# Kernel tuning notes

Hardware: AMD Instinct MI355X
Metric: run time of the kernel (lower is better)

Reference implementation:

```python
import jax, jax.numpy as jnp
import numpy as np

N, IN, HID, OUT, HEADS = 50000, 128, 128, 16, 4
EL, EG = 800000, 200000
NEG_SLOPE = 0.2


def setup_inputs() -> dict:
    key = jax.random.key(0)
    ks = jax.random.split(key, 24)
    def gn(k, shape, fan_in):
        return (jax.random.normal(k, shape, jnp.float32) / np.sqrt(fan_in)).astype(jnp.float32)
    inp = {}
    inp['x'] = jax.random.normal(ks[0], (N, IN), jnp.float32)
    inp['local_edge_index'] = jax.random.randint(ks[1], (2, EL), 0, N, jnp.int64 if jax.config.jax_enable_x64 else jnp.int32)
    inp['global_edge_index'] = jax.random.randint(ks[2], (2, EG), 0, N, jnp.int64 if jax.config.jax_enable_x64 else jnp.int32)
    # local_processor: Linear(IN, HID)
    inp['W1'] = gn(ks[3], (IN, HID), IN); inp['b1'] = jnp.zeros((HID,), jnp.float32)
    # GCNConv(HID, HID): weight + bias
    inp['Wg'] = gn(ks[4], (HID, HID), HID); inp['bg'] = jnp.zeros((HID,), jnp.float32)
    # GATConv(HID, HID, heads=4, concat=False): lin to HEADS*HID, att vectors, bias of size HID
    inp['Wa'] = gn(ks[5], (HID, HEADS * HID), HID)
    inp['att_src'] = gn(ks[6], (HEADS, HID), HID)
    inp['att_dst'] = gn(ks[7], (HEADS, HID), HID)
    inp['ba'] = jnp.zeros((HID,), jnp.float32)
    # hierarchical_pool: Linear(2*HID, HID)
    inp['Wp'] = gn(ks[8], (2 * HID, HID), 2 * HID); inp['bp'] = jnp.zeros((HID,), jnp.float32)
    # classifier: Linear(HID, HID//2) -> ReLU -> Linear(HID//2, OUT)
    inp['Wc1'] = gn(ks[9], (HID, HID // 2), HID); inp['bc1'] = jnp.zeros((HID // 2,), jnp.float32)
    inp['Wc2'] = gn(ks[10], (HID // 2, OUT), HID // 2); inp['bc2'] = jnp.zeros((OUT,), jnp.float32)
    # uncertainty_head: Linear(HID, OUT)
    inp['Wu'] = gn(ks[11], (HID, OUT), HID); inp['bu'] = jnp.zeros((OUT,), jnp.float32)
    return inp


def _add_self_loops(ei, n):
    loop = jnp.arange(n, dtype=ei.dtype)
    return jnp.concatenate([ei[0], loop]), jnp.concatenate([ei[1], loop])


def gcn_conv(x, ei, W, b):
    n = x.shape[0]
    xw = x @ W                                        # [N, HID]
    src, dst = _add_self_loops(ei, n)
    deg = jax.ops.segment_sum(jnp.ones_like(dst, dtype=xw.dtype), dst, num_segments=n)
    dinv = jax.lax.rsqrt(jnp.maximum(deg, 1e-12))     # deg >= 1 thanks to self-loops
    norm = dinv[src] * dinv[dst]                      # [E+N]
    msg = xw[src] * norm[:, None]                     # gather + scale
    return jax.ops.segment_sum(msg, dst, num_segments=n) + b


def gat_conv(x, ei, W, att_src, att_dst, b):
    n = x.shape[0]
    h, c = att_src.shape
    xw = (x @ W).reshape(n, h, c)                     # [N, H, C]
    a_s = jnp.einsum('nhc,hc->nh', xw, att_src)       # [N, H]
    a_d = jnp.einsum('nhc,hc->nh', xw, att_dst)
    src, dst = _add_self_loops(ei, n)
    e = jax.nn.leaky_relu(a_s[src] + a_d[dst], NEG_SLOPE)   # [E+N, H]
    emax = jax.ops.segment_max(e, dst, num_segments=n)      # stable edge-softmax per dst
    ee = jnp.exp(e - emax[dst])
    denom = jax.ops.segment_sum(ee, dst, num_segments=n)
    alpha = ee / (denom[dst] + 1e-16)                        # [E+N, H]
    out = jax.ops.segment_sum(xw[src] * alpha[:, :, None], dst, num_segments=n)  # [N,H,C]
    return out.mean(axis=1) + b                              # concat=False -> head mean


def reference(x, local_edge_index, global_edge_index, W1, b1, Wg, bg, Wa, att_src, att_dst, ba, Wp, bp, Wc1, bc1, Wc2, bc2, Wu, bu):
    x_local = jax.nn.relu(x @ W1 + b1)                       # dropout is identity in eval
    x_lg = jax.nn.relu(gcn_conv(x_local, local_edge_index, Wg, bg))
    x_gg = jax.nn.relu(gat_conv(x_local, global_edge_index, Wa, att_src, att_dst, ba))
    x_comb = jnp.concatenate([x_lg, x_gg], axis=1)           # [N, 2*HID]
    x_pooled = jax.nn.relu(x_comb @ Wp + bp)
    x_final = x_pooled.mean(axis=0, keepdims=True)           # batch=None path
    prediction = jax.nn.relu(x_final @ Wc1 + bc1) @ Wc2 + bc2
    uncertainty = jax.nn.sigmoid(x_final @ Wu + bu)
    return prediction, uncertainty
```

## Files before the change

kernel.cpp:

```cpp
#include <hip/hip_runtime.h>
#include <hip/hip_bf16.h>

#define N_NODES 50000
#define F_IN 128
#define HID 128
#define N_OUT 16
#define HEADS 4
#define EL 800000
#define EG 200000
#define NEG_SLOPE 0.2f
#define NB 196
#define GB 391

typedef short bf16x8 __attribute__((ext_vector_type(8)));
typedef float f32x4 __attribute__((ext_vector_type(4)));
typedef float f32x2 __attribute__((ext_vector_type(2)));

static __device__ __forceinline__ float lrelu(float x) {
    return x > 0.f ? x : NEG_SLOPE * x;
}
static __device__ __forceinline__ unsigned short f2b(float f) {
    __hip_bfloat16 h = __float2bfloat16(f);
    return *reinterpret_cast<unsigned short*>(&h);
}
static __device__ __forceinline__ unsigned char f2fp8(float f) {
    unsigned pk = __builtin_amdgcn_cvt_pk_fp8_f32(f, f, 0, false);
    return (unsigned char)(pk & 0xFF);
}
static __device__ __forceinline__ f32x2 fp8x2_to_f32(unsigned u) {
    return __builtin_amdgcn_cvt_pk_f32_fp8((int)u, false);
}
static __device__ __forceinline__ float rdlane_f(float v, int l) {
    return __int_as_float(__builtin_amdgcn_readlane(__float_as_int(v), l));
}

__global__ __launch_bounds__(256) void conv_hist(
    const float* __restrict__ W1, unsigned short* __restrict__ W1t,
    const float* __restrict__ Wg, unsigned short* __restrict__ Wgt,
    const float* __restrict__ Wa, unsigned short* __restrict__ Wat,
    const float* __restrict__ Wp, unsigned short* __restrict__ Wpt,
    const int* __restrict__ ldst, const int* __restrict__ gdst, int* __restrict__ ghist)
{
    int b = blockIdx.x, t = threadIdx.x;
    if (b < 64) {
        int idx = b * 256 + t;
        int k = idx >> 7, n = idx & 127;
        W1t[n * 128 + k] = f2b(W1[idx]);
    } else if (b < 128) {
        int idx = (b - 64) * 256 + t;
        int k = idx >> 7, n = idx & 127;
        Wgt[n * 128 + k] = f2b(Wg[idx]);
    } else if (b < 384) {
        int idx = (b - 128) * 256 + t;
        int k = idx >> 9, n = idx & 511;
        Wat[(size_t)n * 128 + k] = f2b(Wa[idx]);
    } else if (b < 512) {
        int idx = (b - 384) * 256 + t;
        int k = idx >> 7, n = idx & 127;
        Wpt[(size_t)n * 256 + k] = f2b(Wp[idx]);
    } else {
        __shared__ int lh[NB];
        int blk = b - 512;
        bool loc = blk < 196;
        const int* dstp = loc ? ldst : gdst;
        int nE = loc ? EL : EG;
        int* gh = ghist + (loc ? 0 : NB);
        int start = (loc ? blk : blk - 196) * 4096;
        if (t < NB) lh[t] = 0;
        __syncthreads();
        #pragma unroll
        for (int i = 0; i < 16; i++) {
            int e = start + i * 256 + t;
            if (e < nE) atomicAdd(&lh[dstp[e] >> 8], 1);
        }
        __syncthreads();
        if (t < NB && lh[t]) atomicAdd(&gh[t], lh[t]);
    }
}

__global__ __launch_bounds__(256) void scan_gemmx(
    const int* __restrict__ ghist, int* __restrict__ bbase, int* __restrict__ gcur,
    const float* __restrict__ A, const unsigned short* __restrict__ Bt,
    const float* __restrict__ bias, unsigned short* __restrict__ out, int M)
{
    __shared__ unsigned short As[128 * 128];
    __shared__ unsigned short Bs[128 * 128];
    int tid = threadIdx.x;
    if (blockIdx.x < 2) {
        int* s = (int*)As;
        int g = blockIdx.x, t = tid;
        int v = (t < NB) ? ghist[g * NB + t] : 0;
        s[t] = v;
        __syncthreads();
        for (int off = 1; off < 256; off <<= 1) {
            int u = (t >= off) ? s[t - off] : 0;
            __syncthreads();
            s[t] += u;
            __syncthreads();
        }
        if (t < NB) {
            bbase[g * (NB + 1) + t] = s[t] - v;
            gcur[g * NB + t] = s[t] - v;
        }
        if (t == NB - 1) bbase[g * (NB + 1) + NB] = s[t];
        return;
    }
    int lane = tid & 63, w = tid >> 6;
    int wr = w >> 1, wc = w & 1;
    int l16 = lane & 15, lhi = lane >> 4;
    int m0 = (blockIdx.x - 2) * 128;
    f32x4 acc[4][4] = {};
    #pragma unroll
    for (int i = 0; i < 8; i++) {
        int u = tid + i * 256;
        int row = u >> 4, e0 = (u & 15) << 3;
        int sw = e0 ^ ((row & 7) << 3);
        int gr = m0 + row;
        unsigned short pb[8] = {};
        if (gr < M) {
            float4 a0 = *(const float4*)(A + (size_t)gr * 128 + e0);
            float4 a1 = *(const float4*)(A + (size_t)gr * 128 + e0 + 4);
            pb[0] = f2b(a0.x); pb[1] = f2b(a0.y); pb[2] = f2b(a0.z); pb[3] = f2b(a0.w);
            pb[4] = f2b(a1.x); pb[5] = f2b(a1.y); pb[6] = f2b(a1.z); pb[7] = f2b(a1.w);
        }
        *(bf16x8*)(As + row * 128 + sw) = *(bf16x8*)pb;
        bf16x8 vb = *(const bf16x8*)(Bt + (size_t)row * 128 + e0);
        *(bf16x8*)(Bs + row * 128 + sw) = vb;
    }
    __syncthreads();
    #pragma unroll
    for (int kk = 0; kk < 4; kk++) {
        int ke = kk * 32 + lhi * 8;
        bf16x8 af[4], bfr[4];
        #pragma unroll
        for (int m = 0; m < 4; m++) {
            int r = wr * 64 + m * 16 + l16;
            af[m] = *(const bf16x8*)(As + r * 128 + (ke ^ ((r & 7) << 3)));
        }
        #pragma unroll
        for (int n = 0; n < 4; n++) {
            int r = wc * 64 + n * 16 + l16;
            bfr[n] = *(const bf16x8*)(Bs + r * 128 + (ke ^ ((r & 7) << 3)));
        }
        #pragma unroll
        for (int m = 0; m < 4; m++)
            #pragma unroll
            for (int n = 0; n < 4; n++)
                acc[m][n] = __builtin_amdgcn_mfma_f32_16x16x32_bf16(af[m], bfr[n], acc[m][n], 0, 0, 0);
    }
    #pragma unroll
    for (int m = 0; m < 4; m++) {
        #pragma unroll
        for (int r = 0; r < 4; r++) {
            int row_g = m0 + wr * 64 + m * 16 + lhi * 4 + r;
            if (row_g >= M) continue;
            #pragma unroll
            for (int n = 0; n < 4; n++) {
                int col_g = wc * 64 + n * 16 + l16;
                float v = fmaxf(acc[m][n][r] + bias[col_g], 0.f);
                out[(size_t)row_g * 128 + col_g] = f2b(v);
            }
        }
    }
}

__global__ __launch_bounds__(256) void part_gw5(
    const unsigned short* __restrict__ A, const unsigned short* __restrict__ Wgt,
    const unsigned short* __restrict__ Wat,
    unsigned char* __restrict__ xw_g8, unsigned char* __restrict__ xw_a8, int M,
    const float* __restrict__ atts, const float* __restrict__ attd,
    float* __restrict__ a_s, float* __restrict__ a_d,
    const int* __restrict__ lsrc, const int* __restrict__ ldst,
    const int* __restrict__ gsrc, const int* __restrict__ gdst,
    int* __restrict__ gcur, unsigned* __restrict__ ebuf_l, unsigned* __restrict__ ebuf_g)
{
    __shared__ unsigned short As[128 * 128];
    __shared__ unsigned short Bs[128 * 128];
    __shared__ float sas[128], sad[128];
    int tid = threadIdx.x;
    if (blockIdx.x >= GB) {
        int* lhist = (int*)As;
        int* lbase = ((int*)As) + 256;
        int blk = blockIdx.x - GB, t = tid;
        bool loc = blk < 196;
        const int* srcp = loc ? lsrc : gsrc;
        const int* dstp = loc ? ldst : gdst;
        int nE = loc ? EL : EG;
        unsigned* ebuf = loc ? ebuf_l : ebuf_g;
        int* cur = gcur + (loc ? 0 : NB);
        int start = (loc ? blk : blk - 196) * 4096;
        if (t < NB) lhist[t] = 0;
        __syncthreads();
        unsigned pk[16];
        #pragma unroll
        for (int i = 0; i < 16; i++) {
            int e = start + i * 256 + t;
            if (e < nE) {
                unsigned d = (unsigned)dstp[e];
                pk[i] = (d << 16) | (unsigned)srcp[e];
                atomicAdd(&lhist[d >> 8], 1);
            } else pk[i] = 0xFFFFFFFFu;
        }
        __syncthreads();
        if (t < NB) lbase[t] = atomicAdd(&cur[t], lhist[t]);
        __syncthreads();
        if (t < NB) lhist[t] = 0;
        __syncthreads();
        #pragma unroll
        for (int i = 0; i < 16; i++) {
            unsigned b = pk[i] >> 24;
            if (b < NB) {
                int r = atomicAdd(&lhist[b], 1);
                ebuf[lbase[b] + r] = pk[i];
            }
        }
        return;
    }
    int lane = tid & 63, w = tid >> 6;
    int wr = w >> 1, wc = w & 1;
    int l16 = lane & 15, lhi = lane >> 4;
    int m0 = blockIdx.x * 128;
    #pragma unroll
    for (int i = 0; i < 8; i++) {
        int u = tid + i * 256;
        int row = u >> 4, e0 = (u & 15) << 3;
        int sw = e0 ^ ((row & 7) << 3);
        bf16x8 va = {};
        int gr = m0 + row;
        if (gr < M) va = *(const bf16x8*)(A + (size_t)gr * 128 + e0);
        *(bf16x8*)(As + row * 128 + sw) = va;
    }
    for (int p = 0; p < 5; p++) {
        const unsigned short* Bt = (p == 0) ? Wgt : (Wat + (size_t)(p - 1) * 128 * 128);
        __syncthreads();
        #pragma unroll
        for (int i = 0; i < 8; i++) {
            int u = tid + i * 256;
            int row = u >> 4, e0 = (u & 15) << 3;
            int sw = e0 ^ ((row & 7) << 3);
            bf16x8 vb = *(const bf16x8*)(Bt + (size_t)row * 128 + e0);
            *(bf16x8*)(Bs + row * 128 + sw) = vb;
        }
        if (tid < 128) { sas[tid] = 0.f; sad[tid] = 0.f; }
        __syncthreads();
        f32x4 acc[4][4] = {};
        #pragma unroll
        for (int kk = 0; kk < 4; kk++) {
            int ke = kk * 32 + lhi * 8;
            bf16x8 af[4], bfr[4];
            #pragma unroll
            for (int m = 0; m < 4; m++) {
                int r = wr * 64 + m * 16 + l16;
                af[m] = *(const bf16x8*)(As + r * 128 + (ke ^ ((r & 7) << 3)));
            }
            #pragma unroll
            for (int n = 0; n < 4; n++) {
                int r = wc * 64 + n * 16 + l16;
                bfr[n] = *(const bf16x8*)(Bs + r * 128 + (ke ^ ((r & 7) << 3)));
            }
            #pragma unroll
            for (int m = 0; m < 4; m++)
                #pragma unroll
                for (int n = 0; n < 4; n++)
                    acc[m][n] = __builtin_amdgcn_mfma_f32_16x16x32_bf16(af[m], bfr[n], acc[m][n], 0, 0, 0);
        }
        if (p == 0) {
            #pragma unroll
            for (int m = 0; m < 4; m++)
                #pragma unroll
                for (int r = 0; r < 4; r++) {
                    int row_g = m0 + wr * 64 + m * 16 + lhi * 4 + r;
                    if (row_g >= M) continue;
                    #pragma unroll
                    for (int n = 0; n < 4; n++) {
                        int col_g = wc * 64 + n * 16 + l16;
                        xw_g8[(size_t)row_g * 128 + col_g] = f2fp8(acc[m][n][r]);
                    }
                }
        } else {
            int head = p - 1;
            float ats[4], atd[4];
            #pragma unroll
            for (int n = 0; n < 4; n++) {
                int cl = wc * 64 + n * 16 + l16;
                ats[n] = atts[head * 128 + cl];
                atd[n] = attd[head * 128 + cl];
            }
            #pragma unroll
            for (int m = 0; m < 4; m++) {
                #pragma unroll
                for (int r = 0; r < 4; r++) {
                    int row_l = wr * 64 + m * 16 + lhi * 4 + r;
                    int row_g = m0 + row_l;
                    float ps = 0.f, pd = 0.f;
                    #pragma unroll
                    for (int n = 0; n < 4; n++) {
                        float v = acc[m][n][r];
                        ps = fmaf(v, ats[n], ps);
                        pd = fmaf(v, atd[n], pd);
                        if (row_g < M) {
                            int col_g = head * 128 + wc * 64 + n * 16 + l16;
                            xw_a8[(size_t)row_g * 512 + col_g] = f2fp8(v);
                        }
                    }
                    #pragma unroll
                    for (int off = 1; off < 16; off <<= 1) {
                        ps += __shfl_xor(ps, off);
                        pd += __shfl_xor(pd, off);
                    }
                    if (l16 == 0) {
                        atomicAdd(&sas[row_l], ps);
                        atomicAdd(&sad[row_l], pd);
                    }
                }
            }
            __syncthreads();
            if (tid < 128) {
                int row_g = m0 + tid;
                if (row_g < M) {
                    a_s[(size_t)row_g * 4 + head] = sas[tid];
                    a_d[(size_t)row_g * 4 + head] = sad[tid];
                }
            }
        }
    }
}

__global__ __launch_bounds__(256) void bucket_csr(
    const unsigned* __restrict__ ebuf_l, const unsigned* __restrict__ ebuf_g,
    const int* __restrict__ bbase,
    int* __restrict__ offs_l, int* __restrict__ offs_g,
    unsigned short* __restrict__ csr_l, unsigned short* __restrict__ csr_g,
    float* __restrict__ dinv, unsigned* __restrict__ xwg32)
{
    __shared__ int cnt[256], s[256], cur[256];
    __shared__ float sdinv[256];
    int blk = blockIdx.x, t = threadIdx.x;
    bool loc = blk < 196;
    int b = loc ? blk : blk - 196;
    const unsigned* ebuf = loc ? ebuf_l : ebuf_g;
    const int* bb = bbase + (loc ? 0 : NB + 1);
    int* offs = loc ? offs_l : offs_g;
    unsigned short* csr = loc ? csr_l : csr_g;
    int rs = bb[b], re = bb[b + 1];
    cnt[t] = 0;
    __syncthreads();
    for (int i = rs + t; i < re; i += 256) atomicAdd(&cnt[(ebuf[i] >> 16) & 255], 1);
    __syncthreads();
    int v = cnt[t];
    s[t] = v;
    __syncthreads();
    for (int off = 1; off < 256; off <<= 1) {
        int u = (t >= off) ? s[t - off] : 0;
        __syncthreads();
        s[t] += u;
        __syncthreads();
    }
    int excl = s[t] - v;
    int node = b * 256 + t;
    cur[t] = rs + excl;
    float dv = rsqrtf((float)(v + 1));
    if (node < N_NODES) {
        offs[node] = rs + excl;
        if (loc) dinv[node] = dv;
    }
    sdinv[t] = dv;
    if (blk == 0 && t == 0) offs_l[N_NODES] = EL;
    if (blk == 196 && t == 0) offs_g[N_NODES] = EG;
    __syncthreads();
    for (int i = rs + t; i < re; i += 256) {
        unsigned pk = ebuf[i];
        int r = atomicAdd(&cur[(pk >> 16) & 255], 1);
        csr[r] = (unsigned short)(pk & 0xFFFFu);
    }
    if (loc) {
        size_t base_u = (size_t)b * 256 * 32;
        for (int u = t; u < 256 * 32; u += 256) {
            int nl = u >> 5;
            int nodeg = b * 256 + nl;
            if (nodeg >= N_NODES) break;
            unsigned wv = xwg32[base_u + u];
            f32x2 lo = __builtin_amdgcn_cvt_pk_f32_fp8((int)wv, false);
            f32x2 hi = __builtin_amdgcn_cvt_pk_f32_fp8((int)wv, true);
            float dvn = sdinv[nl];
            lo *= dvn; hi *= dvn;
            unsigned pk2 = __builtin_amdgcn_cvt_pk_fp8_f32(lo[0], lo[1], 0, false);
            pk2 = __builtin_amdgcn_cvt_pk_fp8_f32(hi[0], hi[1], pk2, true);
            xwg32[base_u + u] = pk2;
        }
    }
}

__global__ __launch_bounds__(256) void fused_gather(
    const int* __restrict__ offs_l, const unsigned short* __restrict__ csr_l,
    const unsigned char* __restrict__ xw_g8, const float* __restrict__ dinv,
    const float* __restrict__ bg,
    const int* __restrict__ offs_g, const unsigned short* __restrict__ csr_g,
    const float* __restrict__ a_s, const float* __restrict__ a_d,
    const unsigned char* __restrict__ xw_a8, const float* __restrict__ ba,
    unsigned short* __restrict__ xcomb)
{
    int blk = blockIdx.x;
    int tid = threadIdx.x;
    int lane = tid & 63;
    int g = lane >> 4, q = lane & 15;
    if (blk < 12500) {
        int d = (blk * 256 + tid) >> 6;
        if (d >= N_NODES) return;
        int base = offs_l[d], end = offs_l[d + 1];
        unsigned goff = (unsigned)q * 8u;
        f32x2 a0 = {0.f, 0.f}, a1 = {0.f, 0.f}, a2 = {0.f, 0.f}, a3 = {0.f, 0.f};
        for (int i = base; i < end; ) {
            int chunk = min(64, end - i);
            int sv = (lane < chunk) ? (int)csr_l[i + lane] : 0;
            int nst = (chunk + 3) >> 2;
            int j = 0;
            for (; j + 2 <= nst; j += 2) {
                int eA = j * 4 + g, eB = eA + 4;
                int sA = __shfl(sv, eA);
                int sB = __shfl(sv, eB);
                float mkA = (eA < chunk) ? 1.f : 0.f;
                float mkB = (eB < chunk) ? 1.f : 0.f;
                uint2 vA = *(const uint2*)(xw_g8 + (((unsigned)sA) << 7) + goff);
                uint2 vB = *(const uint2*)(xw_g8 + (((unsigned)sB) << 7) + goff);
                f32x2 mA = {mkA, mkA}, mB = {mkB, mkB};
                a0 += __builtin_amdgcn_cvt_pk_f32_fp8((int)vA.x, false) * mA;
                a1 += __builtin_amdgcn_cvt_pk_f32_fp8((int)vA.x, true) * mA;
                a2 += __builtin_amdgcn_cvt_pk_f32_fp8((int)vA.y, false) * mA;
                a3 += __builtin_amdgcn_cvt_pk_f32_fp8((int)vA.y, true) * mA;
                a0 += __builtin_amdgcn_cvt_pk_f32_fp8((int)vB.x, false) * mB;
                a1 += __builtin_amdgcn_cvt_pk_f32_fp8((int)vB.x, true) * mB;
                a2 += __builtin_amdgcn_cvt_pk_f32_fp8((int)vB.y, false) * mB;
                a3 += __builtin_amdgcn_cvt_pk_f32_fp8((int)vB.y, true) * mB;
            }
            for (; j < nst; j++) {
                int e = j * 4 + g;
                int s = __shfl(sv, e);
                float mk = (e < chunk) ? 1.f : 0.f;
                f32x2 m2 = {mk, mk};
                uint2 v = *(const uint2*)(xw_g8 + (((unsigned)s) << 7) + goff);
                a0 += __builtin_amdgcn_cvt_pk_f32_fp8((int)v.x, false) * m2;
                a1 += __builtin_amdgcn_cvt_pk_f32_fp8((int)v.x, true) * m2;
                a2 += __builtin_amdgcn_cvt_pk_f32_fp8((int)v.y, false) * m2;
                a3 += __builtin_amdgcn_cvt_pk_f32_fp8((int)v.y, true) * m2;
            }
            i += chunk;
        }
        float av[8] = {a0[0], a0[1], a1[0], a1[1], a2[0], a2[1], a3[0], a3[1]};
        #pragma unroll
        for (int k = 0; k < 8; k++) {
            av[k] += __shfl_xor(av[k], 16);
            av[k] += __shfl_xor(av[k], 32);
        }
        if (g == 0) {
            float dd = dinv[d];
            uint2 sv2 = *(const uint2*)(xw_g8 + (((unsigned)d) << 7) + goff);
            f32x2 s0 = fp8x2_to_f32(sv2.x & 0xFFFFu);
            f32x2 s1 = __builtin_amdgcn_cvt_pk_f32_fp8((int)sv2.x, true);
            f32x2 s2 = fp8x2_to_f32(sv2.y & 0xFFFFu);
            f32x2 s3 = __builtin_amdgcn_cvt_pk_f32_fp8((int)sv2.y, true);
            float sf[8] = {s0[0], s0[1], s1[0], s1[1], s2[0], s2[1], s3[0], s3[1]};
            float4 b0 = *(const float4*)(bg + q * 8);
            float4 b1 = *(const float4*)(bg + q * 8 + 4);
            float bb[8] = {b0.x, b0.y, b0.z, b0.w, b1.x, b1.y, b1.z, b1.w};
            unsigned o[4];
            #pragma unroll
            for (int k = 0; k < 4; k++) {
                float v0 = fmaxf(dd * (av[2 * k] + sf[2 * k]) + bb[2 * k], 0.f);
                float v1 = fmaxf(dd * (av[2 * k + 1] + sf[2 * k + 1]) + bb[2 * k + 1], 0.f);
                o[k] = (unsigned)f2b(v0) | ((unsigned)f2b(v1) << 16);
            }
            *(uint4*)(xcomb + (size_t)d * 256 + q * 8) = make_uint4(o[0], o[1], o[2], o[3]);
        }
    } else {
        int d = ((blk - 12500) * 256 + tid) >> 6;
        if (d >= N_NODES) return;
        int base = offs_g[d], end = offs_g[d + 1];
        int deg = end - base;
        if (deg <= 16) {
            float ad_g = a_d[(size_t)d * 4 + g];
            float es = lrelu(a_s[(size_t)d * 4 + g] + ad_g);
            int sv = (q < deg) ? (int)csr_g[base + q] : 0;
            float asg = a_s[(size_t)sv * 4 + g];
            float e = (q < deg) ? lrelu(asg + ad_g) : -1e30f;
            float m = e;
            m = fmaxf(m, __shfl_xor(m, 1));
            m = fmaxf(m, __shfl_xor(m, 2));
            m = fmaxf(m, __shfl_xor(m, 4));
            m = fmaxf(m, __shfl_xor(m, 8));
            m = fmaxf(m, es);
            float wgt = (q < deg) ? __expf(e - m) : 0.f;
            float den = wgt;
            den += __shfl_xor(den, 1);
            den += __shfl_xor(den, 2);
            den += __shfl_xor(den, 4);
            den += __shfl_xor(den, 8);
            float se = __expf(es - m);
            den += se;
            float rinv = 0.25f / (den + 1e-16f);
            float wf = wgt * rinv;
            float selfw = se * rinv;
            unsigned goff = (unsigned)(g * 128 + q * 8);
            int b48 = lane & 48;
            f32x2 a0 = {0.f, 0.f}, a1 = {0.f, 0.f}, a2 = {0.f, 0.f}, a3 = {0.f, 0.f};
            int j = 0;
            for (; j + 2 <= deg; j += 2) {
                int sA = __builtin_amdgcn_readlane(sv, j);
                int sB = __builtin_amdgcn_readlane(sv, j + 1);
                float alA = __shfl(wf, b48 + j);
                float alB = __shfl(wf, b48 + j + 1);
                uint2 vA = *(const uint2*)(xw_a8 + (((unsigned)sA) << 9) + goff);
                uint2 vB = *(const uint2*)(xw_a8 + (((unsigned)sB) << 9) + goff);
                f32x2 mA = {alA, alA}, mB = {alB, alB};
                a0 += __builtin_amdgcn_cvt_pk_f32_fp8((int)vA.x, false) * mA;
                a1 += __builtin_amdgcn_cvt_pk_f32_fp8((int)vA.x, true) * mA;
                a2 += __builtin_amdgcn_cvt_pk_f32_fp8((int)vA.y, false) * mA;
                a3 += __builtin_amdgcn_cvt_pk_f32_fp8((int)vA.y, true) * mA;
                a0 += __builtin_amdgcn_cvt_pk_f32_fp8((int)vB.x, false) * mB;
                a1 += __builtin_amdgcn_cvt_pk_f32_fp8((int)vB.x, true) * mB;
                a2 += __builtin_amdgcn_cvt_pk_f32_fp8((int)vB.y, false) * mB;
                a3 += __builtin_amdgcn_cvt_pk_f32_fp8((int)vB.y, true) * mB;
            }
            if (j < deg) {
                int sA = __builtin_amdgcn_readlane(sv, j);
                float alA = __shfl(wf, b48 + j);
                uint2 vA = *(const uint2*)(xw_a8 + (((unsigned)sA) << 9) + goff);
                f32x2 mA = {alA, alA};
                a0 += __builtin_amdgcn_cvt_pk_f32_fp8((int)vA.x, false) * mA;
                a1 += __builtin_amdgcn_cvt_pk_f32_fp8((int)vA.x, true) * mA;
                a2 += __builtin_amdgcn_cvt_pk_f32_fp8((int)vA.y, false) * mA;
                a3 += __builtin_amdgcn_cvt_pk_f32_fp8((int)vA.y, true) * mA;
            }
            {
                uint2 v = *(const uint2*)(xw_a8 + (((unsigned)d) << 9) + goff);
                f32x2 ms = {selfw, selfw};
                a0 += __builtin_amdgcn_cvt_pk_f32_fp8((int)v.x, false) * ms;
                a1 += __builtin_amdgcn_cvt_pk_f32_fp8((int)v.x, true) * ms;
                a2 += __builtin_amdgcn_cvt_pk_f32_fp8((int)v.y, false) * ms;
                a3 += __builtin_amdgcn_cvt_pk_f32_fp8((int)v.y, true) * ms;
            }
            float av[8] = {a0[0], a0[1], a1[0], a1[1], a2[0], a2[1], a3[0], a3[1]};
            #pragma unroll
            for (int k = 0; k < 8; k++) {
                av[k] += __shfl_xor(av[k], 16);
                av[k] += __shfl_xor(av[k], 32);
            }
            if (g == 0) {
                float4 b0 = *(const float4*)(ba + q * 8);
                float4 b1 = *(const float4*)(ba + q * 8 + 4);
                float bb[8] = {b0.x, b0.y, b0.z, b0.w, b1.x, b1.y, b1.z, b1.w};
                unsigned o[4];
                #pragma unroll
                for (int k = 0; k < 4; k++) {
                    float v0 = fmaxf(av[2 * k] + bb[2 * k], 0.f);
                    float v1 = fmaxf(av[2 * k + 1] + bb[2 * k + 1], 0.f);
                    o[k] = (unsigned)f2b(v0) | ((unsigned)f2b(v1) << 16);
                }
                *(uint4*)(xcomb + (size_t)d * 256 + 128 + q * 8) = make_uint4(o[0], o[1], o[2], o[3]);
            }
            return;
        }
        float4 ad4 = *(const float4*)(a_d + (size_t)d * 4);
        float4 asd = *(const float4*)(a_s + (size_t)d * 4);
        float es0 = lrelu(asd.x + ad4.x), es1 = lrelu(asd.y + ad4.y);
        float es2 = lrelu(asd.z + ad4.z), es3 = lrelu(asd.w + ad4.w);
        if (deg <= 64) {
            int sv = 0;
            float e0 = -1e30f, e1 = -1e30f, e2 = -1e30f, e3 = -1e30f;
            if (lane < deg) {
                sv = csr_g[base + lane];
                float4 s4 = *(const float4*)(a_s + (size_t)sv * 4);
                e0 = lrelu(s4.x + ad4.x); e1 = lrelu(s4.y + ad4.y);
                e2 = lrelu(s4.z + ad4.z); e3 = lrelu(s4.w + ad4.w);
            }
            float m0 = e0, m1 = e1, m2 = e2, m3 = e3;
            #pragma unroll
            for (int off = 1; off < 64; off <<= 1) {
                m0 = fmaxf(m0, __shfl_xor(m0, off));
                m1 = fmaxf(m1, __shfl_xor(m1, off));
                m2 = fmaxf(m2, __shfl_xor(m2, off));
                m3 = fmaxf(m3, __shfl_xor(m3, off));
            }
            m0 = fmaxf(m0, es0); m1 = fmaxf(m1, es1);
            m2 = fmaxf(m2, es2); m3 = fmaxf(m3, es3);
            float w0 = (lane < deg) ? __expf(e0 - m0) : 0.f;
            float w1 = (lane < deg) ? __expf(e1 - m1) : 0.f;
            float w2 = (lane < deg) ? __expf(e2 - m2) : 0.f;
            float w3 = (lane < deg) ? __expf(e3 - m3) : 0.f;
            float d0 = w0, d1 = w1, d2 = w2, d3 = w3;
            #pragma unroll
            for (int off = 1; off < 64; off <<= 1) {
                d0 += __shfl_xor(d0, off); d1 += __shfl_xor(d1, off);
                d2 += __shfl_xor(d2, off); d3 += __shfl_xor(d3, off);
            }
            d0 += __expf(es0 - m0); d1 += __expf(es1 - m1);
            d2 += __expf(es2 - m2); d3 += __expf(es3 - m3);
            float r0 = 0.25f / (d0 + 1e-16f), r1 = 0.25f / (d1 + 1e-16f);
            float r2 = 0.25f / (d2 + 1e-16f), r3 = 0.25f / (d3 + 1e-16f);
            w0 *= r0; w1 *= r1; w2 *= r2; w3 *= r3;
            float wsel = (g == 0) ? w0 : (g == 1) ? w1 : (g == 2) ? w2 : w3;
            float selfw = (g == 0) ? __expf(es0 - m0) * r0 : (g == 1) ? __expf(es1 - m1) * r1
                        : (g == 2) ? __expf(es2 - m2) * r2 : __expf(es3 - m3) * r3;
            unsigned goff = (unsigned)(g * 128 + q * 8);
            f32x2 a0 = {0.f, 0.f}, a1 = {0.f, 0.f}, a2 = {0.f, 0.f}, a3 = {0.f, 0.f};
            for (int j = 0; j < deg; j++) {
                int s = __builtin_amdgcn_readlane(sv, j);
                float al = rdlane_f(wsel, j);
                uint2 v = *(const uint2*)(xw_a8 + (((unsigned)s) << 9) + goff);
                f32x2 mA = {al, al};
                a0 += __builtin_amdgcn_cvt_pk_f32_fp8((int)v.x, false) * mA;
                a1 += __builtin_amdgcn_cvt_pk_f32_fp8((int)v.x, true) * mA;
                a2 += __builtin_amdgcn_cvt_pk_f32_fp8((int)v.y, false) * mA;
                a3 += __builtin_amdgcn_cvt_pk_f32_fp8((int)v.y, true) * mA;
            }
            {
                uint2 v = *(const uint2*)(xw_a8 + (((unsigned)d) << 9) + goff);
                f32x2 ms = {selfw, selfw};
                a0 += __builtin_amdgcn_cvt_pk_f32_fp8((int)v.x, false) * ms;
                a1 += __builtin_amdgcn_cvt_pk_f32_fp8((int)v.x, true) * ms;
                a2 += __builtin_amdgcn_cvt_pk_f32_fp8((int)v.y, false) * ms;
                a3 += __builtin_amdgcn_cvt_pk_f32_fp8((int)v.y, true) * ms;
            }
            float av[8] = {a0[0], a0[1], a1[0], a1[1], a2[0], a2[1], a3[0], a3[1]};
            #pragma unroll
            for (int k = 0; k < 8; k++) {
                av[k] += __shfl_xor(av[k], 16);
                av[k] += __shfl_xor(av[k], 32);
            }
            if (g == 0) {
                float4 b0 = *(const float4*)(ba + q * 8);
                float4 b1 = *(const float4*)(ba + q * 8 + 4);
                float bb[8] = {b0.x, b0.y, b0.z, b0.w, b1.x, b1.y, b1.z, b1.w};
                unsigned o[4];
                #pragma unroll
                for (int k = 0; k < 4; k++) {
                    float v0 = fmaxf(av[2 * k] + bb[2 * k], 0.f);
                    float v1 = fmaxf(av[2 * k + 1] + bb[2 * k + 1], 0.f);
                    o[k] = (unsigned)f2b(v0) | ((unsigned)f2b(v1) << 16);
                }
                *(uint4*)(xcomb + (size_t)d * 256 + 128 + q * 8) = make_uint4(o[0], o[1], o[2], o[3]);
            }
        } else {
            int c2 = lane * 2;
            const unsigned short* xa = (const unsigned short*)xw_a8;
            float m0 = es0, m1 = es1, m2 = es2, m3 = es3;
            for (int i = base; i < end; i += 64) {
                int c = min(64, end - i);
                float t0 = -1e30f, t1 = -1e30f, t2 = -1e30f, t3 = -1e30f;
                if (lane < c) {
                    int s = csr_g[i + lane];
                    float4 s4 = *(const float4*)(a_s + (size_t)s * 4);
                    t0 = lrelu(s4.x + ad4.x); t1 = lrelu(s4.y + ad4.y);
                    t2 = lrelu(s4.z + ad4.z); t3 = lrelu(s4.w + ad4.w);
                }
                m0 = fmaxf(m0, t0); m1 = fmaxf(m1, t1);
                m2 = fmaxf(m2, t2); m3 = fmaxf(m3, t3);
            }
            #pragma unroll
            for (int off = 1; off < 64; off <<= 1) {
                m0 = fmaxf(m0, __shfl_xor(m0, off));
                m1 = fmaxf(m1, __shfl_xor(m1, off));
                m2 = fmaxf(m2, __shfl_xor(m2, off));
                m3 = fmaxf(m3, __shfl_xor(m3, off));
            }
            float d0 = 0.f, d1 = 0.f, d2 = 0.f, d3 = 0.f;
            for (int i = base; i < end; i += 64) {
                int c = min(64, end - i);
                if (lane < c) {
                    int s = csr_g[i + lane];
                    float4 s4 = *(const float4*)(a_s + (size_t)s * 4);
                    d0 += __expf(lrelu(s4.x + ad4.x) - m0);
                    d1 += __expf(lrelu(s4.y + ad4.y) - m1);
                    d2 += __expf(lrelu(s4.z + ad4.z) - m2);
                    d3 += __expf(lrelu(s4.w + ad4.w) - m3);
                }
            }
            #pragma unroll
            for (int off = 1; off < 64; off <<= 1) {
                d0 += __shfl_xor(d0, off); d1 += __shfl_xor(d1, off);
                d2 += __shfl_xor(d2, off); d3 += __shfl_xor(d3, off);
            }
            d0 += __expf(es0 - m0); d1 += __expf(es1 - m1);
            d2 += __expf(es2 - m2); d3 += __expf(es3 - m3);
            float r0 = 1.f / (d0 + 1e-16f), r1 = 1.f / (d1 + 1e-16f);
            float r2 = 1.f / (d2 + 1e-16f), r3 = 1.f / (d3 + 1e-16f);
            float ax = 0.f, ay = 0.f;
            for (int i = base; i < end; i += 64) {
                int c = min(64, end - i);
                int sv = 0;
                float w0 = 0.f, w1 = 0.f, w2 = 0.f, w3 = 0.f;
                if (lane < c) {
                    sv = csr_g[i + lane];
                    float4 s4 = *(const float4*)(a_s + (size_t)sv * 4);
                    w0 = __expf(lrelu(s4.x + ad4.x) - m0) * r0;
                    w1 = __expf(lrelu(s4.y + ad4.y) - m1) * r1;
                    w2 = __expf(lrelu(s4.z + ad4.z) - m2) * r2;
                    w3 = __expf(lrelu(s4.w + ad4.w) - m3) * r3;
                }
                for (int j = 0; j < c; j++) {
                    int s = __shfl(sv, j);
                    float a0 = __shfl(w0, j), a1 = __shfl(w1, j);
                    float a2 = __shfl(w2, j), a3 = __shfl(w3, j);
                    const unsigned short* row = xa + (size_t)s * 256 + lane;
                    f32x2 v0 = fp8x2_to_f32(row[0]);
                    f32x2 v1 = fp8x2_to_f32(row[64]);
                    f32x2 v2 = fp8x2_to_f32(row[128]);
                    f32x2 v3 = fp8x2_to_f32(row[192]);
                    ax = fmaf(v0[0], a0, ax); ay = fmaf(v0[1], a0, ay);
                    ax = fmaf(v1[0], a1, ax); ay = fmaf(v1[1], a1, ay);
                    ax = fmaf(v2[0], a2, ax); ay = fmaf(v2[1], a2, ay);
                    ax = fmaf(v3[0], a3, ax); ay = fmaf(v3[1], a3, ay);
                }
            }
            float s0 = __expf(es0 - m0) * r0, s1 = __expf(es1 - m1) * r1;
            float s2 = __expf(es2 - m2) * r2, s3 = __expf(es3 - m3) * r3;
            const unsigned short* row = xa + (size_t)d * 256 + lane;
            f32x2 v0 = fp8x2_to_f32(row[0]);
            f32x2 v1 = fp8x2_to_f32(row[64]);
            f32x2 v2 = fp8x2_to_f32(row[128]);
            f32x2 v3 = fp8x2_to_f32(row[192]);
            ax = fmaf(v0[0], s0, ax); ay = fmaf(v0[1], s0, ay);
            ax = fmaf(v1[0], s1, ax); ay = fmaf(v1[1], s1, ay);
            ax = fmaf(v2[0], s2, ax); ay = fmaf(v2[1], s2, ay);
            ax = fmaf(v3[0], s3, ax); ay = fmaf(v3[1], s3, ay);
            float ox = fmaxf(0.25f * ax + ba[c2], 0.f);
            float oy = fmaxf(0.25f * ay + ba[c2 + 1], 0.f);
            unsigned uo = (unsigned)f2b(ox) | ((unsigned)f2b(oy) << 16);
            *(unsigned*)(xcomb + (size_t)d * 256 + 128 + c2) = uo;
        }
    }
}

__global__ __launch_bounds__(256) void mfma_pool_head(
    const unsigned short* __restrict__ A, const unsigned short* __restrict__ Bt,
    const float* __restrict__ bp, float* __restrict__ sumvec, int* __restrict__ counter,
    int M,
    const float* __restrict__ Wc1, const float* __restrict__ bc1,
    const float* __restrict__ Wc2, const float* __restrict__ bc2,
    const float* __restrict__ Wu, const float* __restrict__ bu,
    float* __restrict__ out)
{
    __shared__ unsigned short As[128 * 128];
    __shared__ unsigned short Bs[128 * 128];
    __shared__ float red[128];
    __shared__ int lastflag;
    int tid = threadIdx.x;
    int lane = tid & 63, w = tid >> 6;
    int wr = w >> 1, wc = w & 1;
    int l16 = lane & 15, lhi = lane >> 4;
    int m0 = blockIdx.x * 128;
    f32x4 acc[4][4] = {};
    for (int kb = 0; kb < 256; kb += 128) {
        if (kb) __syncthreads();
        #pragma unroll
        for (int i = 0; i < 8; i++) {
            int u = tid + i * 256;
            int row = u >> 4, e0 = (u & 15) << 3;
            int sw = e0 ^ ((row & 7) << 3);
            bf16x8 va = {};
            int gr = m0 + row;
            if (gr < M) va = *(const bf16x8*)(A + (size_t)gr * 256 + kb + e0);
            *(bf16x8*)(As + row * 128 + sw) = va;
            bf16x8 vb = *(const bf16x8*)(Bt + (size_t)row * 256 + kb + e0);
            *(bf16x8*)(Bs + row * 128 + sw) = vb;
        }
        __syncthreads();
        #pragma unroll
        for (int kk = 0; kk < 4; kk++) {
            int ke = kk * 32 + lhi * 8;
            bf16x8 af[4], bfr[4];
            #pragma unroll
            for (int m = 0; m < 4; m++) {
                int r = wr * 64 + m * 16 + l16;
                af[m] = *(const bf16x8*)(As + r * 128 + (ke ^ ((r & 7) << 3)));
            }
            #pragma unroll
            for (int n = 0; n < 4; n++) {
                int r = wc * 64 + n * 16 + l16;
                bfr[n] = *(const bf16x8*)(Bs + r * 128 + (ke ^ ((r & 7) << 3)));
            }
            #pragma unroll
            for (int m = 0; m < 4; m++)
                #pragma unroll
                for (int n = 0; n < 4; n++)
                    acc[m][n] = __builtin_amdgcn_mfma_f32_16x16x32_bf16(af[m], bfr[n], acc[m][n], 0, 0, 0);
        }
    }
    float bcol[4];
    #pragma unroll
    for (int n = 0; n < 4; n++) bcol[n] = bp[wc * 64 + n * 16 + l16];
    float colsum[4] = {0.f, 0.f, 0.f, 0.f};
    #pragma unroll
    for (int m = 0; m < 4; m++) {
        #pragma unroll
        for (int r = 0; r < 4; r++) {
            int row_g = m0 + wr * 64 + m * 16 + lhi * 4 + r;
            if (row_g < M) {
                #pragma unroll
                for (int n = 0; n < 4; n++)
                    colsum[n] += fmaxf(acc[m][n][r] + bcol[n], 0.f);
            }
        }
    }
    #pragma unroll
    for (int n = 0; n < 4; n++) {
        colsum[n] += __shfl_xor(colsum[n], 16);
        colsum[n] += __shfl_xor(colsum[n], 32);
    }
    if (tid < 128) red[tid] = 0.f;
    __syncthreads();
    if (lhi == 0) {
        #pragma unroll
        for (int n = 0; n < 4; n++)
            atomicAdd(&red[wc * 64 + n * 16 + l16], colsum[n]);
    }
    __syncthreads();
    if (tid < 128) atomicAdd(&sumvec[tid], red[tid]);
    __threadfence();
    __syncthreads();
    if (tid == 0) lastflag = (atomicAdd(counter, 1) == (int)gridDim.x - 1);
    __syncthreads();
    if (!lastflag) return;
    __shared__ float xf[128];
    __shared__ float h1[64];
    if (tid < 128) xf[tid] = atomicAdd(&sumvec[tid], 0.f) * (1.0f / N_NODES);
    __syncthreads();
    if (tid < 64) {
        float s = bc1[tid];
        for (int c = 0; c < 128; c++) s = fmaf(xf[c], Wc1[c * 64 + tid], s);
        h1[tid] = fmaxf(s, 0.f);
    }
    __syncthreads();
    if (tid < 16) {
        float s = bc2[tid];
        for (int j = 0; j < 64; j++) s = fmaf(h1[j], Wc2[j * 16 + tid], s);
        out[tid] = s;
        float u = bu[tid];
        for (int c = 0; c < 128; c++) u = fmaf(xf[c], Wu[c * 16 + tid], u);
        out[16 + tid] = 1.0f / (1.0f + expf(-u));
    }
}

extern "C" void kernel_launch(void* const* d_in, const int* in_sizes, int n_in,
                              void* d_out, int out_size, void* d_ws, size_t ws_size,
                              hipStream_t stream) {
    const float* x    = (const float*)d_in[0];
    const int*   lei  = (const int*)d_in[1];
    const int*   gei  = (const int*)d_in[2];
    const float* W1   = (const float*)d_in[3];
    const float* b1   = (const float*)d_in[4];
    const float* Wg   = (const float*)d_in[5];
    const float* bg   = (const float*)d_in[6];
    const float* Wa   = (const float*)d_in[7];
    const float* atts = (const float*)d_in[8];
    const float* attd = (const float*)d_in[9];
    const float* ba   = (const float*)d_in[10];
    const float* Wp   = (const float*)d_in[11];
    const float* bp   = (const float*)d_in[12];
    const float* Wc1  = (const float*)d_in[13];
    const float* bc1  = (const float*)d_in[14];
    const float* Wc2  = (const float*)d_in[15];
    const float* bc2  = (const float*)d_in[16];
    const float* Wu   = (const float*)d_in[17];
    const float* bu   = (const float*)d_in[18];

    const int* lsrc = lei;
    const int* ldst = lei + EL;
    const int* gsrc = gei;
    const int* gdst = gei + EG;

    uintptr_t base = (uintptr_t)d_ws;
    auto alloc = [&](size_t bytes) { void* p = (void*)base; base += (bytes + 255) & ~(size_t)255; return p; };
    unsigned short* x_loc  = (unsigned short*)alloc((size_t)N_NODES * 128 * 2);
    unsigned char*  xw_g8  = (unsigned char*)alloc((size_t)N_NODES * 128);
    unsigned char*  xw_a8  = (unsigned char*)alloc((size_t)N_NODES * 512);
    unsigned short* xcomb  = (unsigned short*)alloc((size_t)N_NODES * 256 * 2);
    unsigned short* W1t    = (unsigned short*)alloc((size_t)128 * 128 * 2);
    unsigned short* Wgt    = (unsigned short*)alloc((size_t)128 * 128 * 2);
    unsigned short* Wat    = (unsigned short*)alloc((size_t)512 * 128 * 2);
    unsigned short* Wpt    = (unsigned short*)alloc((size_t)128 * 256 * 2);
    float* dinv       = (float*)alloc((size_t)N_NODES * 4);
    float* a_s        = (float*)alloc((size_t)N_NODES * 4 * 4);
    float* a_d        = (float*)alloc((size_t)N_NODES * 4 * 4);
    int*   ghist      = (int*)alloc((size_t)2 * NB * 4);
    int*   bbase      = (int*)alloc((size_t)2 * (NB + 1) * 4);
    int*   gcur       = (int*)alloc((size_t)2 * NB * 4);
    unsigned* ebuf_l  = (unsigned*)alloc((size_t)EL * 4);
    unsigned* ebuf_g  = (unsigned*)alloc((size_t)EG * 4);
    int*   offs_l     = (int*)alloc(((size_t)N_NODES + 1) * 4);
    int*   offs_g     = (int*)alloc(((size_t)N_NODES + 1) * 4);
    unsigned short* csr_l = (unsigned short*)alloc((size_t)EL * 2);
    unsigned short* csr_g = (unsigned short*)alloc((size_t)EG * 2);
    float* sumvec     = (float*)alloc(128 * 4 + 256);
    int*   counter    = (int*)(sumvec + 128);

    hipMemsetAsync(ghist, 0, (size_t)2 * NB * 4, stream);
    hipMemsetAsync(sumvec, 0, 128 * 4 + 4, stream);

    conv_hist<<<757, 256, 0, stream>>>(W1, W1t, Wg, Wgt, Wa, Wat, Wp, Wpt,
                                       ldst, gdst, ghist);
    scan_gemmx<<<393, 256, 0, stream>>>(ghist, bbase, gcur, x, W1t, b1, x_loc, N_NODES);
    part_gw5<<<GB + 245, 256, 0, stream>>>(x_loc, Wgt, Wat, xw_g8, xw_a8, N_NODES,
                                           atts, attd, a_s, a_d,
                                           lsrc, ldst, gsrc, gdst, gcur, ebuf_l, ebuf_g);
    bucket_csr<<<392, 256, 0, stream>>>(ebuf_l, ebuf_g, bbase, offs_l, offs_g,
                                        csr_l, csr_g, dinv, (unsigned*)xw_g8);
    fused_gather<<<25000, 256, 0, stream>>>(offs_l, csr_l, xw_g8, dinv, bg,
                                            offs_g, csr_g, a_s, a_d, xw_a8, ba, xcomb);
    mfma_pool_head<<<GB, 256, 0, stream>>>(xcomb, Wpt, bp, sumvec, counter, N_NODES,
                                           Wc1, bc1, Wc2, bc2, Wu, bu, (float*)d_out);
}
```

Baseline: 206.7 us.

## Split bucket partition from GEMM and fold dinv scaling into GEMM epilogue

Edge bucket partitioning moves out of the fused GEMM launch into its own kernel, and the CSR build now runs before the GEMM. The GEMM can therefore read dinv and scale xw_g in its epilogue before fp8 quantization. This removes the separate read-dequantize-scale-requantize pass over xw_g8 in bucket_csr and one fp8 rounding step. The cost is one extra kernel launch, and the partition blocks can no longer overlap with the GEMM blocks.

```diff
diff --git a/kernel.cpp b/kernel.cpp
--- a/kernel.cpp
+++ b/kernel.cpp
@@ -164,58 +164,105 @@
     }
 }
 
-__global__ __launch_bounds__(256) void part_gw5(
+__global__ __launch_bounds__(256) void bucket_part(
+    const int* __restrict__ lsrc, const int* __restrict__ ldst,
+    const int* __restrict__ gsrc, const int* __restrict__ gdst,
+    int* __restrict__ gcur, unsigned* __restrict__ ebuf_l, unsigned* __restrict__ ebuf_g)
+{
+    __shared__ int lhist[NB], lbase[NB];
+    int blk = blockIdx.x, t = threadIdx.x;
+    bool loc = blk < 196;
+    const int* srcp = loc ? lsrc : gsrc;
+    const int* dstp = loc ? ldst : gdst;
+    int nE = loc ? EL : EG;
+    unsigned* ebuf = loc ? ebuf_l : ebuf_g;
+    int* cur = gcur + (loc ? 0 : NB);
+    int start = (loc ? blk : blk - 196) * 4096;
+    if (t < NB) lhist[t] = 0;
+    __syncthreads();
+    unsigned pk[16];
+    #pragma unroll
+    for (int i = 0; i < 16; i++) {
+        int e = start + i * 256 + t;
+        if (e < nE) {
+            unsigned d = (unsigned)dstp[e];
+            pk[i] = (d << 16) | (unsigned)srcp[e];
+            atomicAdd(&lhist[d >> 8], 1);
+        } else pk[i] = 0xFFFFFFFFu;
+    }
+    __syncthreads();
+    if (t < NB) lbase[t] = atomicAdd(&cur[t], lhist[t]);
+    __syncthreads();
+    if (t < NB) lhist[t] = 0;
+    __syncthreads();
+    #pragma unroll
+    for (int i = 0; i < 16; i++) {
+        unsigned b = pk[i] >> 24;
+        if (b < NB) {
+            int r = atomicAdd(&lhist[b], 1);
+            ebuf[lbase[b] + r] = pk[i];
+        }
+    }
+}
+
+__global__ __launch_bounds__(256) void bucket_csr(
+    const unsigned* __restrict__ ebuf_l, const unsigned* __restrict__ ebuf_g,
+    const int* __restrict__ bbase,
+    int* __restrict__ offs_l, int* __restrict__ offs_g,
+    unsigned short* __restrict__ csr_l, unsigned short* __restrict__ csr_g,
+    float* __restrict__ dinv)
+{
+    __shared__ int cnt[256], s[256], cur[256];
+    int blk = blockIdx.x, t = threadIdx.x;
+    bool loc = blk < 196;
+    int b = loc ? blk : blk - 196;
+    const unsigned* ebuf = loc ? ebuf_l : ebuf_g;
+    const int* bb = bbase + (loc ? 0 : NB + 1);
+    int* offs = loc ? offs_l : offs_g;
+    unsigned short* csr = loc ? csr_l : csr_g;
+    int rs = bb[b], re = bb[b + 1];
+    cnt[t] = 0;
+    __syncthreads();
+    for (int i = rs + t; i < re; i += 256) atomicAdd(&cnt[(ebuf[i] >> 16) & 255], 1);
+    __syncthreads();
+    int v = cnt[t];
+    s[t] = v;
+    __syncthreads();
+    for (int off = 1; off < 256; off <<= 1) {
+        int u = (t >= off) ? s[t - off] : 0;
+        __syncthreads();
+        s[t] += u;
+        __syncthreads();
+    }
+    int excl = s[t] - v;
+    int node = b * 256 + t;
+    cur[t] = rs + excl;
+    if (node < N_NODES) {
+        offs[node] = rs + excl;
+        if (loc) dinv[node] = rsqrtf((float)(v + 1));
+    }
+    if (blk == 0 && t == 0) offs_l[N_NODES] = EL;
+    if (blk == 196 && t == 0) offs_g[N_NODES] = EG;
+    __syncthreads();
+    for (int i = rs + t; i < re; i += 256) {
+        unsigned pk = ebuf[i];
+        int r = atomicAdd(&cur[(pk >> 16) & 255], 1);
+        csr[r] = (unsigned short)(pk & 0xFFFFu);
+    }
+}
+
+__global__ __launch_bounds__(256) void gemm_gw5(
     const unsigned short* __restrict__ A, const unsigned short* __restrict__ Wgt,
     const unsigned short* __restrict__ Wat,
     unsigned char* __restrict__ xw_g8, unsigned char* __restrict__ xw_a8, int M,
     const float* __restrict__ atts, const float* __restrict__ attd,
     float* __restrict__ a_s, float* __restrict__ a_d,
-    const int* __restrict__ lsrc, const int* __restrict__ ldst,
-    const int* __restrict__ gsrc, const int* __restrict__ gdst,
-    int* __restrict__ gcur, unsigned* __restrict__ ebuf_l, unsigned* __restrict__ ebuf_g)
+    const float* __restrict__ dinv)
 {
     __shared__ unsigned short As[128 * 128];
     __shared__ unsigned short Bs[128 * 128];
     __shared__ float sas[128], sad[128];
     int tid = threadIdx.x;
-    if (blockIdx.x >= GB) {
-        int* lhist = (int*)As;
-        int* lbase = ((int*)As) + 256;
-        int blk = blockIdx.x - GB, t = tid;
-        bool loc = blk < 196;
-        const int* srcp = loc ? lsrc : gsrc;
-        const int* dstp = loc ? ldst : gdst;
-        int nE = loc ? EL : EG;
-        unsigned* ebuf = loc ? ebuf_l : ebuf_g;
-        int* cur = gcur + (loc ? 0 : NB);
-        int start = (loc ? blk : blk - 196) * 4096;
-        if (t < NB) lhist[t] = 0;
-        __syncthreads();
-        unsigned pk[16];
-        #pragma unroll
-        for (int i = 0; i < 16; i++) {
-            int e = start + i * 256 + t;
-            if (e < nE) {
-                unsigned d = (unsigned)dstp[e];
-                pk[i] = (d << 16) | (unsigned)srcp[e];
-                atomicAdd(&lhist[d >> 8], 1);
-            } else pk[i] = 0xFFFFFFFFu;
-        }
-        __syncthreads();
-        if (t < NB) lbase[t] = atomicAdd(&cur[t], lhist[t]);
-        __syncthreads();
-        if (t < NB) lhist[t] = 0;
-        __syncthreads();
-        #pragma unroll
-        for (int i = 0; i < 16; i++) {
-            unsigned b = pk[i] >> 24;
-            if (b < NB) {
-                int r = atomicAdd(&lhist[b], 1);
-                ebuf[lbase[b] + r] = pk[i];
-            }
-        }
-        return;
-    }
     int lane = tid & 63, w = tid >> 6;
     int wr = w >> 1, wc = w & 1;
     int l16 = lane & 15, lhi = lane >> 4;
@@ -271,10 +318,11 @@
                 for (int r = 0; r < 4; r++) {
                     int row_g = m0 + wr * 64 + m * 16 + lhi * 4 + r;
                     if (row_g >= M) continue;
+                    float dv = dinv[row_g];
                     #pragma unroll
                     for (int n = 0; n < 4; n++) {
                         int col_g = wc * 64 + n * 16 + l16;
-                        xw_g8[(size_t)row_g * 128 + col_g] = f2fp8(acc[m][n][r]);
+                        xw_g8[(size_t)row_g * 128 + col_g] = f2fp8(acc[m][n][r] * dv);
                     }
                 }
         } else {
@@ -322,71 +370,6 @@
                     a_d[(size_t)row_g * 4 + head] = sad[tid];
                 }
             }
-        }
-    }
-}
-
-__global__ __launch_bounds__(256) void bucket_csr(
-    const unsigned* __restrict__ ebuf_l, const unsigned* __restrict__ ebuf_g,
-    const int* __restrict__ bbase,
-    int* __restrict__ offs_l, int* __restrict__ offs_g,
-    unsigned short* __restrict__ csr_l, unsigned short* __restrict__ csr_g,
-    float* __restrict__ dinv, unsigned* __restrict__ xwg32)
-{
-    __shared__ int cnt[256], s[256], cur[256];
-    __shared__ float sdinv[256];
-    int blk = blockIdx.x, t = threadIdx.x;
-    bool loc = blk < 196;
-    int b = loc ? blk : blk - 196;
-    const unsigned* ebuf = loc ? ebuf_l : ebuf_g;
-    const int* bb = bbase + (loc ? 0 : NB + 1);
-    int* offs = loc ? offs_l : offs_g;
-    unsigned short* csr = loc ? csr_l : csr_g;
-    int rs = bb[b], re = bb[b + 1];
-    cnt[t] = 0;
-    __syncthreads();
-    for (int i = rs + t; i < re; i += 256) atomicAdd(&cnt[(ebuf[i] >> 16) & 255], 1);
-    __syncthreads();
-    int v = cnt[t];
-    s[t] = v;
-    __syncthreads();
-    for (int off = 1; off < 256; off <<= 1) {
-        int u = (t >= off) ? s[t - off] : 0;
-        __syncthreads();
-        s[t] += u;
-        __syncthreads();
-    }
-    int excl = s[t] - v;
-    int node = b * 256 + t;
-    cur[t] = rs + excl;
-    float dv = rsqrtf((float)(v + 1));
-    if (node < N_NODES) {
-        offs[node] = rs + excl;
-        if (loc) dinv[node] = dv;
-    }
-    sdinv[t] = dv;
-    if (blk == 0 && t == 0) offs_l[N_NODES] = EL;
-    if (blk == 196 && t == 0) offs_g[N_NODES] = EG;
-    __syncthreads();
-    for (int i = rs + t; i < re; i += 256) {
-        unsigned pk = ebuf[i];
-        int r = atomicAdd(&cur[(pk >> 16) & 255], 1);
-        csr[r] = (unsigned short)(pk & 0xFFFFu);
-    }
-    if (loc) {
-        size_t base_u = (size_t)b * 256 * 32;
-        for (int u = t; u < 256 * 32; u += 256) {
-            int nl = u >> 5;
-            int nodeg = b * 256 + nl;
-            if (nodeg >= N_NODES) break;
-            unsigned wv = xwg32[base_u + u];
-            f32x2 lo = __builtin_amdgcn_cvt_pk_f32_fp8((int)wv, false);
-            f32x2 hi = __builtin_amdgcn_cvt_pk_f32_fp8((int)wv, true);
-            float dvn = sdinv[nl];
-            lo *= dvn; hi *= dvn;
-            unsigned pk2 = __builtin_amdgcn_cvt_pk_fp8_f32(lo[0], lo[1], 0, false);
-            pk2 = __builtin_amdgcn_cvt_pk_fp8_f32(hi[0], hi[1], pk2, true);
-            xwg32[base_u + u] = pk2;
         }
     }
 }
@@ -900,11 +883,11 @@
     conv_hist<<<757, 256, 0, stream>>>(W1, W1t, Wg, Wgt, Wa, Wat, Wp, Wpt,
                                        ldst, gdst, ghist);
     scan_gemmx<<<393, 256, 0, stream>>>(ghist, bbase, gcur, x, W1t, b1, x_loc, N_NODES);
-    part_gw5<<<GB + 245, 256, 0, stream>>>(x_loc, Wgt, Wat, xw_g8, xw_a8, N_NODES,
-                                           atts, attd, a_s, a_d,
-                                           lsrc, ldst, gsrc, gdst, gcur, ebuf_l, ebuf_g);
+    bucket_part<<<245, 256, 0, stream>>>(lsrc, ldst, gsrc, gdst, gcur, ebuf_l, ebuf_g);
     bucket_csr<<<392, 256, 0, stream>>>(ebuf_l, ebuf_g, bbase, offs_l, offs_g,
-                                        csr_l, csr_g, dinv, (unsigned*)xw_g8);
+                                        csr_l, csr_g, dinv);
+    gemm_gw5<<<GB, 256, 0, stream>>>(x_loc, Wgt, Wat, xw_g8, xw_a8, N_NODES,
+                                     atts, attd, a_s, a_d, dinv);
     fused_gather<<<25000, 256, 0, stream>>>(offs_l, csr_l, xw_g8, dinv, bg,
                                             offs_g, csr_g, a_s, a_d, xw_a8, ba, xcomb);
     mfma_pool_head<<<GB, 256, 0, stream>>>(xcomb, Wpt, bp, sumvec, counter, N_NODES,
```

Result: faster. 187.2 us (-9.4%).
